# Optimization experiments

Measured on AMD Instinct MI355X. Metric: run time of the kernel, lower is better.

The kernel has to match this reference:

```python
import jax, jax.numpy as jnp
import numpy as np

B, N, D, H = 32, 2048, 65, 64  # batch, seq_len, in_dim+out_dim, hid
GAMMA = 0.0001


def setup_inputs() -> dict:
    key = jax.random.key(0)
    kx, kq, kk, kv = jax.random.split(key, 4)
    x = jax.random.normal(kx, (B, N, D), dtype=jnp.float32)
    std_qk = (GAMMA / D) ** 0.5
    Wq = jax.random.normal(kq, (H, D), dtype=jnp.float32) * std_qk
    Wk = jax.random.normal(kk, (H, D), dtype=jnp.float32) * std_qk
    Wv = jax.random.normal(kv, (D, D), dtype=jnp.float32) * GAMMA
    return {"x": x, "Wq": Wq, "Wk": Wk, "Wv": Wv}


def reference(x, Wq, Wk, Wv):
    # Linear projections (torch nn.Linear: x @ W^T)
    Q = jnp.einsum('bnd,hd->bnh', x, Wq)  # [B, N, H]
    K = jnp.einsum('bnd,hd->bnh', x, Wk)  # [B, N, H]
    V = jnp.einsum('bnd,ed->bne', x, Wv)  # [B, N, D]
    # Non-softmax linear attention: (Q K^T) V, as written in the module
    scores = jnp.einsum('bnh,bmh->bnm', Q, K)  # [B, N, N]
    out = jnp.einsum('bnm,bmd->bnd', scores, V)  # [B, N, D]
    return out
```

## Files before the change

### kernel.cpp

```cpp
#include <hip/hip_runtime.h>

#define BB 32
#define NN 2048
#define DD 65
#define HH 64
#define ST 68
#define TILE (DD * ST)
#define CH 64
#define CROWS 32

__device__ __forceinline__ float4 f4add(float4 a, float4 b) {
  return make_float4(a.x + b.x, a.y + b.y, a.z + b.z, a.w + b.w);
}

#define GL2LDS(g, l)                                             \
  __builtin_amdgcn_global_load_lds(                              \
      (const __attribute__((address_space(1))) void*)(g),        \
      (__attribute__((address_space(3))) void*)(l), 16, 0, 0)

__global__ __launch_bounds__(256, 4) void k1_gram(const float* __restrict__ x,
                                                  float* __restrict__ P) {
  __shared__ __align__(16) float Xl[4][CROWS * ST];
  const int t = (int)threadIdx.x;
  const int w = t >> 6, lane = t & 63;
  const int tx8 = lane & 7, ty8 = lane >> 3;
  const int ch = (int)blockIdx.x * 4 + w;
  const int b = ch >> 6, c = ch & 63;
  const float4* src4 =
      (const float4*)(x + ((size_t)b * NN + (size_t)c * CROWS) * DD);
  float* Xw = Xl[w];

  {
    float4 tmp[9];
#pragma unroll
    for (int q = 0; q < 9; q++) {
      const int i4 = lane + 64 * q;
      if (i4 < 520) tmp[q] = src4[i4];
    }
#pragma unroll
    for (int q = 0; q < 9; q++) {
      const int i4 = lane + 64 * q;
      if (i4 < 520) {
        const int f = 4 * i4;
        const float vv[4] = {tmp[q].x, tmp[q].y, tmp[q].z, tmp[q].w};
#pragma unroll
        for (int j = 0; j < 4; j++) {
          const int r = (f + j) / DD, cc = (f + j) - r * DD;
          Xw[r * ST + cc] = vv[j];
        }
      }
    }
  }

  float g[8][8] = {};
  float f64[8] = {};
  float gcc = 0.f;
  for (int n = 0; n < CROWS; n++) {
    float rowf[8], colf[8];
    *(float4*)&rowf[0] = *(const float4*)&Xw[n * ST + 8 * ty8];
    *(float4*)&rowf[4] = *(const float4*)&Xw[n * ST + 8 * ty8 + 4];
    *(float4*)&colf[0] = *(const float4*)&Xw[n * ST + 8 * tx8];
    *(float4*)&colf[4] = *(const float4*)&Xw[n * ST + 8 * tx8 + 4];
    const float x64 = Xw[n * ST + 64];
#pragma unroll
    for (int r = 0; r < 8; r++)
#pragma unroll
      for (int cc = 0; cc < 8; cc++)
        g[r][cc] = fmaf(rowf[r], colf[cc], g[r][cc]);
#pragma unroll
    for (int cc = 0; cc < 8; cc++) f64[cc] = fmaf(x64, colf[cc], f64[cc]);
    gcc = fmaf(x64, x64, gcc);
  }

  float* Pp = P + (size_t)ch * TILE;
#pragma unroll
  for (int r = 0; r < 8; r++) {
    *(float4*)&Pp[(8 * ty8 + r) * ST + 8 * tx8] = *(float4*)&g[r][0];
    *(float4*)&Pp[(8 * ty8 + r) * ST + 8 * tx8 + 4] = *(float4*)&g[r][4];
  }
  if (ty8 == 0) {
#pragma unroll
    for (int cc = 0; cc < 8; cc++) {
      Pp[64 * ST + 8 * tx8 + cc] = f64[cc];
      Pp[(8 * tx8 + cc) * ST + 64] = f64[cc];
    }
    if (tx8 == 0) Pp[64 * ST + 64] = gcc;
  }
}

__global__ __launch_bounds__(256) void kred(const float* __restrict__ P,
                                            float* __restrict__ G) {
  const int t = (int)threadIdx.x;
  const int blk = (int)blockIdx.x;
  const int b = blk / 5, s = blk - b * 5;
  const int Q = TILE / 4;
  const int i4 = s * 256 + t;
  if (i4 < Q) {
    const float4* Pb = (const float4*)(P + (size_t)b * CH * TILE);
    float4 acc = make_float4(0.f, 0.f, 0.f, 0.f);
#pragma unroll
    for (int grp = 0; grp < 8; grp++) {
      float4 v[8];
#pragma unroll
      for (int cc = 0; cc < 8; cc++)
        v[cc] = Pb[(size_t)(8 * grp + cc) * Q + i4];
#pragma unroll
      for (int stp = 4; stp >= 1; stp >>= 1)
#pragma unroll
        for (int cc = 0; cc < stp; cc++) v[cc] = f4add(v[cc], v[cc + stp]);
      acc = f4add(acc, v[0]);
    }
    ((float4*)(G + (size_t)b * TILE))[i4] = acc;
  }
}

__global__ __launch_bounds__(256) void k2_chain(
    const float* __restrict__ Wq, const float* __restrict__ Wk,
    const float* __restrict__ Wv, const float* __restrict__ G,
    float* __restrict__ Tm) {
  __shared__ __align__(16) float WqL[HH * ST];
  __shared__ __align__(16) float WkL[HH * ST];
  __shared__ __align__(16) float GL[TILE];
  __shared__ __align__(16) float WvT[TILE];
  __shared__ __align__(16) float Mr[8 * ST];
  __shared__ __align__(16) float Rr[8 * ST];

  const int t = (int)threadIdx.x;
  const int tx = t & 31, ty = t >> 5;
  const int blk = (int)blockIdx.x;
  const int b = blk / 9, rg = blk - b * 9;
  const int i = 8 * rg + ty;
  const bool alive = (i < DD);
  const int ic = alive ? i : 0;

  {
    float tq[17], tk[17];
#pragma unroll
    for (int q = 0; q < 17; q++) {
      const int idx = t + 256 * q;
      if (idx < HH * DD) { tq[q] = Wq[idx]; tk[q] = Wk[idx]; }
    }
#pragma unroll
    for (int q = 0; q < 17; q++) {
      const int idx = t + 256 * q;
      if (idx < HH * DD) {
        const int r = idx / DD, cc = idx - r * DD;
        WqL[r * ST + cc] = tq[q];
        WkL[r * ST + cc] = tk[q];
      }
    }
  }
  {
    const float4* Gb4 = (const float4*)(G + (size_t)b * TILE);
    float4 tG[5];
#pragma unroll
    for (int q = 0; q < 5; q++) {
      const int i4 = t + 256 * q;
      if (i4 < TILE / 4) tG[q] = Gb4[i4];
    }
#pragma unroll
    for (int q = 0; q < 5; q++) {
      const int i4 = t + 256 * q;
      if (i4 < TILE / 4) *((float4*)GL + i4) = tG[q];
    }
  }
  {
    float tv[17];
#pragma unroll
    for (int q = 0; q < 17; q++) {
      const int idx = t + 256 * q;
      if (idx < DD * DD) tv[q] = Wv[idx];
    }
#pragma unroll
    for (int q = 0; q < 17; q++) {
      const int idx = t + 256 * q;
      if (idx < DD * DD) {
        const int j = idx / DD, k = idx - j * DD;
        WvT[k * ST + j] = tv[q];
      }
    }
  }
  __syncthreads();

  {
    float m0 = 0.f, m1 = 0.f, m2 = 0.f;
    for (int h = 0; h < HH; h++) {
      const float wq = WqL[h * ST + ic];
      m0 = fmaf(wq, WkL[h * ST + tx], m0);
      m1 = fmaf(wq, WkL[h * ST + tx + 32], m1);
      m2 = fmaf(wq, WkL[h * ST + 64], m2);
    }
    if (alive) {
      Mr[ty * ST + tx] = m0;
      Mr[ty * ST + tx + 32] = m1;
      if (tx == 0) Mr[ty * ST + 64] = m2;
    }
  }
  __syncthreads();

  {
    float r0 = 0.f, r1 = 0.f, r2 = 0.f;
    for (int k = 0; k < DD; k++) {
      const float mm = Mr[ty * ST + k];
      r0 = fmaf(mm, GL[k * ST + tx], r0);
      r1 = fmaf(mm, GL[k * ST + tx + 32], r1);
      r2 = fmaf(mm, GL[k * ST + 64], r2);
    }
    if (alive) {
      Rr[ty * ST + tx] = r0;
      Rr[ty * ST + tx + 32] = r1;
      if (tx == 0) Rr[ty * ST + 64] = r2;
    }
  }
  __syncthreads();

  {
    float t0 = 0.f, t1 = 0.f, t2 = 0.f;
    for (int k = 0; k < DD; k++) {
      const float rv = Rr[ty * ST + k];
      t0 = fmaf(rv, WvT[k * ST + tx], t0);
      t1 = fmaf(rv, WvT[k * ST + tx + 32], t1);
      t2 = fmaf(rv, WvT[k * ST + 64], t2);
    }
    if (alive) {
      float* Tb = Tm + (size_t)b * TILE + (size_t)i * ST;
      Tb[tx] = t0;
      Tb[tx + 32] = t1;
      if (tx == 0) Tb[64] = t2;
    }
  }
}

__global__ __launch_bounds__(256, 4) void k3_out(const float* __restrict__ x,
                                                 const float* __restrict__ Tt,
                                                 float* __restrict__ out) {
  __shared__ __align__(16) float Tl[TILE];
  const int t = (int)threadIdx.x;
  const int w = t >> 6, lane = t & 63;
  const int tx8 = lane & 7, ry4 = lane >> 3;
  const int blk = (int)blockIdx.x;
  const int b = blk >> 4;
  const int c = (blk & 15) * 4 + w;
  const float4* Tg4 = (const float4*)(Tt + (size_t)b * TILE);
  const float* xs = x + ((size_t)b * NN + (size_t)c * CROWS) * DD;

#pragma unroll
  for (int q = 0; q < 4; q++)
    GL2LDS(Tg4 + q * 256 + w * 64 + lane,
           Tl + (size_t)(q * 256 + w * 64) * 4);
  {
    const int s = 1024 + w * 64 + lane;
    if (s < TILE / 4) GL2LDS(Tg4 + s, Tl + (size_t)(1024 + w * 64) * 4);
  }
  __syncthreads();

  const float* xr0 = xs + (size_t)(4 * ry4 + 0) * DD;
  const float* xr1 = xs + (size_t)(4 * ry4 + 1) * DD;
  const float* xr2 = xs + (size_t)(4 * ry4 + 2) * DD;
  const float* xr3 = xs + (size_t)(4 * ry4 + 3) * DD;

  float o[4][8] = {}, o64[4] = {};
  for (int kk = 0; kk < 64; kk += 4) {
    float xa[4][4];
#pragma unroll
    for (int e = 0; e < 4; e++) {
      xa[0][e] = xr0[kk + e];
      xa[1][e] = xr1[kk + e];
      xa[2][e] = xr2[kk + e];
      xa[3][e] = xr3[kk + e];
    }
#pragma unroll
    for (int e = 0; e < 4; e++) {
      const int k = kk + e;
      float tb[8];
      *(float4*)&tb[0] = *(const float4*)&Tl[k * ST + 8 * tx8];
      *(float4*)&tb[4] = *(const float4*)&Tl[k * ST + 8 * tx8 + 4];
      const float t64 = Tl[k * ST + 64];
#pragma unroll
      for (int r = 0; r < 4; r++) {
#pragma unroll
        for (int cc = 0; cc < 8; cc++)
          o[r][cc] = fmaf(xa[r][e], tb[cc], o[r][cc]);
        o64[r] = fmaf(xa[r][e], t64, o64[r]);
      }
    }
  }
  {
    float xk[4];
    xk[0] = xr0[64]; xk[1] = xr1[64]; xk[2] = xr2[64]; xk[3] = xr3[64];
    float tb[8];
    *(float4*)&tb[0] = *(const float4*)&Tl[64 * ST + 8 * tx8];
    *(float4*)&tb[4] = *(const float4*)&Tl[64 * ST + 8 * tx8 + 4];
    const float t64 = Tl[64 * ST + 64];
#pragma unroll
    for (int r = 0; r < 4; r++) {
#pragma unroll
      for (int cc = 0; cc < 8; cc++)
        o[r][cc] = fmaf(xk[r], tb[cc], o[r][cc]);
      o64[r] = fmaf(xk[r], t64, o64[r]);
    }
  }

  float* ob = out + ((size_t)b * NN + (size_t)c * CROWS) * DD;
#pragma unroll
  for (int r = 0; r < 4; r++) {
    const int row = 4 * ry4 + r;
#pragma unroll
    for (int cc = 0; cc < 8; cc++)
      ob[row * DD + 8 * tx8 + cc] = o[r][cc];
  }
  if (tx8 == 0) {
#pragma unroll
    for (int r = 0; r < 4; r++)
      ob[(4 * ry4 + r) * DD + 64] = o64[r];
  }
}

extern "C" void kernel_launch(void* const* d_in, const int* in_sizes, int n_in,
                              void* d_out, int out_size, void* d_ws,
                              size_t ws_size, hipStream_t stream) {
  const float* x = (const float*)d_in[0];
  const float* Wq = (const float*)d_in[1];
  const float* Wk = (const float*)d_in[2];
  const float* Wv = (const float*)d_in[3];
  float* out = (float*)d_out;

  float* P = (float*)d_ws;
  float* G = P + (size_t)BB * CH * TILE;
  float* Tm = G + (size_t)BB * TILE;

  k1_gram<<<BB * CH / 4, 256, 0, stream>>>(x, P);
  kred<<<BB * 5, 256, 0, stream>>>(P, G);
  k2_chain<<<BB * 9, 256, 0, stream>>>(Wq, Wk, Wv, G, Tm);
  k3_out<<<BB * CH / 4, 256, 0, stream>>>(x, Tm, out);
  (void)in_sizes; (void)n_in; (void)out_size; (void)ws_size;
}
```

Before: 121.4 us.

## Use block-wide 64-row Gram tiles and stage output through LDS for coalesced stores

The Gram kernel now uses one block of 256 threads per 64-row chunk instead of one wave per 32-row chunk, with a 4x4 register tile per thread, and reads row factors directly from global memory. This halves the number of partial tiles the reduction kernel must sum. The output kernel now writes results to shared memory first and then copies them out with coalesced float4 stores, in place of strided scalar stores. The cost is fewer registers of reuse per thread in the Gram kernel, an extra block-wide sync, and more shared memory in the output kernel, which may reduce occupancy.

Result: no change. 121.1 us (-0.2%).

```diff
diff --git a/kernel.cpp b/kernel.cpp
--- a/kernel.cpp
+++ b/kernel.cpp
@@ -6,8 +6,7 @@
 #define HH 64
 #define ST 68
 #define TILE (DD * ST)
-#define CH 64
-#define CROWS 32
+#define CC 32
 
 __device__ __forceinline__ float4 f4add(float4 a, float4 b) {
   return make_float4(a.x + b.x, a.y + b.y, a.z + b.z, a.w + b.w);
@@ -20,71 +19,67 @@
 
 __global__ __launch_bounds__(256, 4) void k1_gram(const float* __restrict__ x,
                                                   float* __restrict__ P) {
-  __shared__ __align__(16) float Xl[4][CROWS * ST];
+  __shared__ __align__(16) float Xl[64 * ST];
   const int t = (int)threadIdx.x;
-  const int w = t >> 6, lane = t & 63;
-  const int tx8 = lane & 7, ty8 = lane >> 3;
-  const int ch = (int)blockIdx.x * 4 + w;
-  const int b = ch >> 6, c = ch & 63;
-  const float4* src4 =
-      (const float4*)(x + ((size_t)b * NN + (size_t)c * CROWS) * DD);
-  float* Xw = Xl[w];
-
-  {
-    float4 tmp[9];
-#pragma unroll
-    for (int q = 0; q < 9; q++) {
-      const int i4 = lane + 64 * q;
-      if (i4 < 520) tmp[q] = src4[i4];
-    }
-#pragma unroll
-    for (int q = 0; q < 9; q++) {
-      const int i4 = lane + 64 * q;
-      if (i4 < 520) {
+  const int tx = t & 15, ty = t >> 4;
+  const int blk = (int)blockIdx.x;
+  const int b = blk >> 5, c = blk & 31;
+  const float* src = x + ((size_t)b * NN + (size_t)c * 64) * DD;
+  const float4* src4 = (const float4*)src;
+
+  {
+    float4 tmp[5];
+#pragma unroll
+    for (int q = 0; q < 5; q++) {
+      const int i4 = t + 256 * q;
+      if (i4 < 1040) tmp[q] = src4[i4];
+    }
+#pragma unroll
+    for (int q = 0; q < 5; q++) {
+      const int i4 = t + 256 * q;
+      if (i4 < 1040) {
         const int f = 4 * i4;
         const float vv[4] = {tmp[q].x, tmp[q].y, tmp[q].z, tmp[q].w};
 #pragma unroll
         for (int j = 0; j < 4; j++) {
           const int r = (f + j) / DD, cc = (f + j) - r * DD;
-          Xw[r * ST + cc] = vv[j];
+          Xl[r * ST + cc] = vv[j];
         }
       }
     }
   }
-
-  float g[8][8] = {};
-  float f64[8] = {};
+  __syncthreads();
+
+  float g[4][4] = {};
+  float g64[4] = {};
   float gcc = 0.f;
-  for (int n = 0; n < CROWS; n++) {
-    float rowf[8], colf[8];
-    *(float4*)&rowf[0] = *(const float4*)&Xw[n * ST + 8 * ty8];
-    *(float4*)&rowf[4] = *(const float4*)&Xw[n * ST + 8 * ty8 + 4];
-    *(float4*)&colf[0] = *(const float4*)&Xw[n * ST + 8 * tx8];
-    *(float4*)&colf[4] = *(const float4*)&Xw[n * ST + 8 * tx8 + 4];
-    const float x64 = Xw[n * ST + 64];
-#pragma unroll
-    for (int r = 0; r < 8; r++)
-#pragma unroll
-      for (int cc = 0; cc < 8; cc++)
+  const float* srow = src + 4 * ty;
+#pragma unroll 2
+  for (int n = 0; n < 64; n++) {
+    float rowf[4], colf[4];
+#pragma unroll
+    for (int r = 0; r < 4; r++) rowf[r] = srow[n * DD + r];
+    *(float4*)colf = *(const float4*)&Xl[n * ST + 4 * tx];
+    const float x64 = Xl[n * ST + 64];
+#pragma unroll
+    for (int r = 0; r < 4; r++)
+#pragma unroll
+      for (int cc = 0; cc < 4; cc++)
         g[r][cc] = fmaf(rowf[r], colf[cc], g[r][cc]);
 #pragma unroll
-    for (int cc = 0; cc < 8; cc++) f64[cc] = fmaf(x64, colf[cc], f64[cc]);
+    for (int cc = 0; cc < 4; cc++) g64[cc] = fmaf(x64, colf[cc], g64[cc]);
     gcc = fmaf(x64, x64, gcc);
   }
-
-  float* Pp = P + (size_t)ch * TILE;
-#pragma unroll
-  for (int r = 0; r < 8; r++) {
-    *(float4*)&Pp[(8 * ty8 + r) * ST + 8 * tx8] = *(float4*)&g[r][0];
-    *(float4*)&Pp[(8 * ty8 + r) * ST + 8 * tx8 + 4] = *(float4*)&g[r][4];
-  }
-  if (ty8 == 0) {
-#pragma unroll
-    for (int cc = 0; cc < 8; cc++) {
-      Pp[64 * ST + 8 * tx8 + cc] = f64[cc];
-      Pp[(8 * tx8 + cc) * ST + 64] = f64[cc];
-    }
-    if (tx8 == 0) Pp[64 * ST + 64] = gcc;
+  float* Pp = P + (size_t)blk * TILE;
+#pragma unroll
+  for (int r = 0; r < 4; r++)
+    *(float4*)&Pp[(4 * ty + r) * ST + 4 * tx] = *(float4*)g[r];
+  if (ty == 0) {
+    *(float4*)&Pp[64 * ST + 4 * tx] = *(float4*)g64;
+#pragma unroll
+    for (int cc = 0; cc < 4; cc++)
+      Pp[(4 * tx + cc) * ST + 64] = g64[cc];
+    if (tx == 0) Pp[64 * ST + 64] = gcc;
   }
 }
 
@@ -96,10 +91,10 @@
   const int Q = TILE / 4;
   const int i4 = s * 256 + t;
   if (i4 < Q) {
-    const float4* Pb = (const float4*)(P + (size_t)b * CH * TILE);
+    const float4* Pb = (const float4*)(P + (size_t)b * CC * TILE);
     float4 acc = make_float4(0.f, 0.f, 0.f, 0.f);
 #pragma unroll
-    for (int grp = 0; grp < 8; grp++) {
+    for (int grp = 0; grp < 4; grp++) {
       float4 v[8];
 #pragma unroll
       for (int cc = 0; cc < 8; cc++)
@@ -235,6 +230,7 @@
                                                  const float* __restrict__ Tt,
                                                  float* __restrict__ out) {
   __shared__ __align__(16) float Tl[TILE];
+  __shared__ __align__(16) float Ol[4][32 * DD];
   const int t = (int)threadIdx.x;
   const int w = t >> 6, lane = t & 63;
   const int tx8 = lane & 7, ry4 = lane >> 3;
@@ -242,7 +238,7 @@
   const int b = blk >> 4;
   const int c = (blk & 15) * 4 + w;
   const float4* Tg4 = (const float4*)(Tt + (size_t)b * TILE);
-  const float* xs = x + ((size_t)b * NN + (size_t)c * CROWS) * DD;
+  const float* xs = x + ((size_t)b * NN + (size_t)c * 32) * DD;
 
 #pragma unroll
   for (int q = 0; q < 4; q++)
@@ -301,18 +297,21 @@
     }
   }
 
-  float* ob = out + ((size_t)b * NN + (size_t)c * CROWS) * DD;
+  float* Ow = Ol[w];
 #pragma unroll
   for (int r = 0; r < 4; r++) {
     const int row = 4 * ry4 + r;
 #pragma unroll
     for (int cc = 0; cc < 8; cc++)
-      ob[row * DD + 8 * tx8 + cc] = o[r][cc];
-  }
-  if (tx8 == 0) {
-#pragma unroll
-    for (int r = 0; r < 4; r++)
-      ob[(4 * ry4 + r) * DD + 64] = o64[r];
+      Ow[row * DD + 8 * tx8 + cc] = o[r][cc];
+    if (tx8 == 0) Ow[row * DD + 64] = o64[r];
+  }
+  float4* ob4 = (float4*)(out + ((size_t)b * NN + (size_t)c * 32) * DD);
+  const float4* Ow4 = (const float4*)Ow;
+#pragma unroll
+  for (int q = 0; q < 9; q++) {
+    const int i4 = lane + 64 * q;
+    if (i4 < (32 * DD) / 4) ob4[i4] = Ow4[i4];
   }
 }
 
@@ -326,12 +325,12 @@
   float* out = (float*)d_out;
 
   float* P = (float*)d_ws;
-  float* G = P + (size_t)BB * CH * TILE;
+  float* G = P + (size_t)BB * CC * TILE;
   float* Tm = G + (size_t)BB * TILE;
 
-  k1_gram<<<BB * CH / 4, 256, 0, stream>>>(x, P);
+  k1_gram<<<BB * CC, 256, 0, stream>>>(x, P);
   kred<<<BB * 5, 256, 0, stream>>>(P, G);
   k2_chain<<<BB * 9, 256, 0, stream>>>(Wq, Wk, Wv, G, Tm);
-  k3_out<<<BB * CH / 4, 256, 0, stream>>>(x, Tm, out);
+  k3_out<<<BB * CC / 2, 256, 0, stream>>>(x, Tm, out);
   (void)in_sizes; (void)n_in; (void)out_size; (void)ws_size;
 }
```
